# Performance work log

Hardware: AMD Instinct MI355X
Metric: run time of the kernel (lower is better)

Reference implementation:

```python
import jax, jax.numpy as jnp
import numpy as np

SH_DEGREE = 4
SH_DIM = (SH_DEGREE + 1) ** 2  # 25
SCALE_MIN, SCALE_MAX = 0.01, 100.0
SCALE_PCT = 0.1
SRF, GPP = 1, 1


def sh_basis(d):
    # Real spherical harmonics up to l=4 for unit directions d (..., 3) -> (..., 25)
    x, y, z = d[..., 0], d[..., 1], d[..., 2]
    x2, y2, z2 = x * x, y * y, z * z
    return jnp.stack([
        jnp.full_like(x, 0.2820947918),
        0.4886025119 * y, 0.4886025119 * z, 0.4886025119 * x,
        1.0925484306 * x * y, 1.0925484306 * y * z, 0.3153915653 * (3.0 * z2 - 1.0),
        1.0925484306 * x * z, 0.5462742153 * (x2 - y2),
        0.5900435899 * y * (3.0 * x2 - y2), 2.8906114426 * x * y * z,
        0.4570457995 * y * (5.0 * z2 - 1.0), 0.3731763326 * z * (5.0 * z2 - 3.0),
        0.4570457995 * x * (5.0 * z2 - 1.0), 1.4453057213 * z * (x2 - y2),
        0.5900435899 * x * (x2 - 3.0 * y2),
        2.5033429418 * x * y * (x2 - y2), 1.7701307698 * y * z * (3.0 * x2 - y2),
        0.9461746958 * x * y * (7.0 * z2 - 1.0), 0.6690465436 * y * z * (7.0 * z2 - 3.0),
        0.1057855469 * (35.0 * z2 * z2 - 30.0 * z2 + 3.0),
        0.6690465436 * x * z * (7.0 * z2 - 3.0),
        0.4730873479 * (x2 - y2) * (7.0 * z2 - 1.0),
        1.7701307698 * x * z * (x2 - 3.0 * y2),
        0.6258357354 * (x2 * x2 - 6.0 * x2 * y2 + y2 * y2),
    ], -1)


# Fixed sample directions + inverse basis matrices for per-band SH rotation (Wigner-D via sampling)
_rng = np.random.default_rng(0)
_SAMPLES, _YS_INV = {}, {}
for _l in range(1, SH_DEGREE + 1):
    _v = _rng.normal(size=(2 * _l + 1, 3))
    _v /= np.linalg.norm(_v, axis=-1, keepdims=True)
    _SAMPLES[_l] = _v.astype(np.float32)
    _B = np.asarray(sh_basis(jnp.asarray(_SAMPLES[_l])))[:, _l * _l:(_l + 1) ** 2]  # (n, n) rows=samples
    _YS_INV[_l] = np.linalg.inv(_B.T).astype(np.float32)  # inverse of columns-are-samples matrix


def quat_to_rotmat(q):
    # wxyz convention
    w, x, y, z = q[..., 0], q[..., 1], q[..., 2], q[..., 3]
    r0 = jnp.stack([1 - 2 * (y * y + z * z), 2 * (x * y - w * z), 2 * (x * z + w * y)], -1)
    r1 = jnp.stack([2 * (x * y + w * z), 1 - 2 * (x * x + z * z), 2 * (y * z - w * x)], -1)
    r2 = jnp.stack([2 * (x * z - w * y), 2 * (y * z + w * x), 1 - 2 * (x * x + y * y)], -1)
    return jnp.stack([r0, r1, r2], -2)


def rotate_sh(sh, R_c2w):
    # sh: (B,V,R,srf,gpp,3,25); R_c2w: (B,V,3,3). Block-diagonal per-band rotation.
    outs = [sh[..., :1]]  # l=0 invariant
    for l in range(1, SH_DEGREE + 1):
        lo, hi = l * l, (l + 1) ** 2
        S = jnp.asarray(_SAMPLES[l])  # (n,3)
        drot = jnp.einsum('bvji,nj->bvni', R_c2w, S)  # R^T d_n
        Yrot = jnp.swapaxes(sh_basis(drot)[..., lo:hi], -1, -2)  # (B,V,n,n) columns=samples
        D = jnp.swapaxes(Yrot @ jnp.asarray(_YS_INV[l]), -1, -2)  # coefficient rotation
        outs.append(jnp.einsum('bvmn,bvrsgxn->bvrsgxm', D, sh[..., lo:hi]))
    return jnp.concatenate(outs, -1)


def setup_inputs() -> dict:
    key = jax.random.key(0)
    ks = jax.random.split(key, 8)
    B, V, H, W = 2, 4, 256, 256
    R = H * W
    C = 3 + 4 + 3 * SH_DIM  # 82
    pre_gaussians = jax.random.normal(ks[0], (B, V, R, SRF, C), jnp.float32)
    pixel_centers = jax.random.uniform(ks[1], (B, V, R, SRF, 2), jnp.float32)
    q = jax.random.normal(ks[2], (B, V, 4), jnp.float32)
    q = q / jnp.linalg.norm(q, axis=-1, keepdims=True)
    Rm = quat_to_rotmat(q)
    t = 0.5 * jax.random.normal(ks[3], (B, V, 3), jnp.float32)
    E = jnp.zeros((B, V, 4, 4), jnp.float32)
    E = E.at[..., :3, :3].set(Rm).at[..., :3, 3].set(t).at[..., 3, 3].set(1.0)
    f = 1.0 + 0.2 * jax.random.uniform(ks[4], (B, V, 2), jnp.float32)
    c = 0.5 + 0.02 * jax.random.normal(ks[5], (B, V, 2), jnp.float32)
    K = jnp.zeros((B, V, 3, 3), jnp.float32)
    K = K.at[..., 0, 0].set(f[..., 0]).at[..., 1, 1].set(f[..., 1])
    K = K.at[..., 0, 2].set(c[..., 0]).at[..., 1, 2].set(c[..., 1]).at[..., 2, 2].set(1.0)
    opacities = jax.random.uniform(ks[6], (B, V, R), jnp.float32)
    depths = 0.5 + 9.5 * jax.random.uniform(ks[7], (B, V, R), jnp.float32)
    return {"pre_gaussians": pre_gaussians, "pixel_centers": pixel_centers,
            "extrinsics": E, "intrinsics": K, "opacities": opacities,
            "depths": depths, "img_h": H, "img_w": W}


def reference(pre_gaussians, pixel_centers, extrinsics, intrinsics, opacities, depths, img_h, img_w):
    H, W = img_h, img_w
    B, V, R = pre_gaussians.shape[:3]
    C = pre_gaussians.shape[-1]
    pg = jnp.broadcast_to(pre_gaussians[..., None, :], (B, V, R, SRF, GPP, C))
    pc = jnp.broadcast_to(pixel_centers[..., None, :], (B, V, R, SRF, GPP, 2))
    op = jnp.broadcast_to(opacities[..., None, None], (B, V, R, SRF, GPP))
    dep = jnp.broadcast_to(depths[..., None, None], (B, V, R, SRF, GPP))
    scales_raw, quats, sh = pg[..., :3], pg[..., 3:7], pg[..., 7:]
    scales = (SCALE_MIN + (SCALE_MAX - SCALE_MIN) * jax.nn.sigmoid(scales_raw)) * dep[..., None]
    pixel_size = jnp.array([1.0 / W, 1.0 / H], jnp.float32)
    K2inv = jnp.linalg.inv(intrinsics[..., :2, :2])
    scale_adj = SCALE_PCT * jnp.einsum('bvij,j->bv', K2inv, pixel_size)
    scales = scales * scale_adj[:, :, None, None, None, None]
    quats = quats / jnp.linalg.norm(quats, axis=-1, keepdims=True)
    R_w2c = extrinsics[..., :3, :3]
    R_c2w = jnp.swapaxes(R_w2c, -1, -2)
    Rq = quat_to_rotmat(quats)
    cov = jnp.einsum('...ik,...k,...jk->...ij', Rq, scales * scales, Rq)  # Rq S S^T Rq^T
    cov = jnp.einsum('bvai,bvrsgij,bvcj->bvrsgac', R_c2w, cov, R_c2w)
    Kinv = jnp.linalg.inv(intrinsics)
    xy1 = jnp.concatenate([pc, jnp.ones_like(pc[..., :1])], -1)
    dir_cam = jnp.einsum('bvij,bvrsgj->bvrsgi', Kinv, xy1)
    dir_cam = dir_cam / jnp.linalg.norm(dir_cam, axis=-1, keepdims=True)
    ray_d = jnp.einsum('bvij,bvrsgj->bvrsgi', R_c2w, dir_cam)
    t = extrinsics[..., :3, 3]
    cam_o = -jnp.einsum('bvij,bvj->bvi', R_c2w, t)  # camera center in world
    ray_o = jnp.broadcast_to(cam_o[:, :, None, None, None, :], ray_d.shape)
    means = ray_o + ray_d * dep[..., None]
    sh = sh.reshape(B, V, R, SRF, GPP, 3, SH_DIM)
    sh = rotate_sh(sh, R_c2w)
    return (means, scales, cov, quats, op, sh)
```

## Files before the change

kernel.cpp:

```cpp
#include <hip/hip_runtime.h>

#define VSZ  192
#define TILE 64
#define ROWW 95
#define NTHR 256

__device__ __forceinline__ void sh_basis25(float x, float y, float z, float* Y) {
    float x2 = x * x, y2 = y * y, z2 = z * z;
    Y[0]  = 0.2820947918f;
    Y[1]  = 0.4886025119f * y;
    Y[2]  = 0.4886025119f * z;
    Y[3]  = 0.4886025119f * x;
    Y[4]  = 1.0925484306f * x * y;
    Y[5]  = 1.0925484306f * y * z;
    Y[6]  = 0.3153915653f * (3.0f * z2 - 1.0f);
    Y[7]  = 1.0925484306f * x * z;
    Y[8]  = 0.5462742153f * (x2 - y2);
    Y[9]  = 0.5900435899f * y * (3.0f * x2 - y2);
    Y[10] = 2.8906114426f * x * y * z;
    Y[11] = 0.4570457995f * y * (5.0f * z2 - 1.0f);
    Y[12] = 0.3731763326f * z * (5.0f * z2 - 3.0f);
    Y[13] = 0.4570457995f * x * (5.0f * z2 - 1.0f);
    Y[14] = 1.4453057213f * z * (x2 - y2);
    Y[15] = 0.5900435899f * x * (x2 - 3.0f * y2);
    Y[16] = 2.5033429418f * x * y * (x2 - y2);
    Y[17] = 1.7701307698f * y * z * (3.0f * x2 - y2);
    Y[18] = 0.9461746958f * x * y * (7.0f * z2 - 1.0f);
    Y[19] = 0.6690465436f * y * z * (7.0f * z2 - 3.0f);
    Y[20] = 0.1057855469f * (35.0f * z2 * z2 - 30.0f * z2 + 3.0f);
    Y[21] = 0.6690465436f * x * z * (7.0f * z2 - 3.0f);
    Y[22] = 0.4730873479f * (x2 - y2) * (7.0f * z2 - 1.0f);
    Y[23] = 1.7701307698f * x * z * (x2 - 3.0f * y2);
    Y[24] = 0.6258357354f * (x2 * x2 - 6.0f * x2 * y2 + y2 * y2);
}

__global__ __launch_bounds__(64) void setup_kernel(
        const float* __restrict__ ext,
        const float* __restrict__ intr,
        const int* __restrict__ ph,
        const int* __restrict__ pw,
        float* __restrict__ vdg) {
    __shared__ float Bs[24][9];
    __shared__ float Yrs[24][9];
    __shared__ float normInv[24];

    int bv = blockIdx.x;
    int tid = threadIdx.x;
    const float* E = ext + bv * 16;
    const float* K = intr + bv * 9;
    float* o = vdg + bv * VSZ;

    const float z0 = 0.5f, r0 = 0.8660254037844386f;
    const float TWO_PI = 6.283185307179586f;

    if (tid < 24) {
        int l, base;
        if      (tid < 3)  { l = 1; base = 0;  }
        else if (tid < 8)  { l = 2; base = 3;  }
        else if (tid < 15) { l = 3; base = 8;  }
        else               { l = 4; base = 15; }
        int n  = 2 * l + 1;
        int si = tid - base;
        int lo = l * l;
        float phs = 0.4f + TWO_PI * (float)si / (float)n;
        float sx = r0 * cosf(phs), sy = r0 * sinf(phs), sz = z0;
        float Y[25];
        sh_basis25(sx, sy, sz, Y);
        for (int k = 0; k < n; k++) Bs[tid][k] = Y[lo + k];
        float dx = E[0] * sx + E[1] * sy + E[2]  * sz;
        float dy = E[4] * sx + E[5] * sy + E[6]  * sz;
        float dz = E[8] * sx + E[9] * sy + E[10] * sz;
        sh_basis25(dx, dy, dz, Y);
        for (int k = 0; k < n; k++) Yrs[tid][k] = Y[lo + k];
    }
    __syncthreads();

    if (tid < 24) {
        int l, base;
        if      (tid < 3)  { l = 1; base = 0;  }
        else if (tid < 8)  { l = 2; base = 3;  }
        else if (tid < 15) { l = 3; base = 8;  }
        else               { l = 4; base = 15; }
        int n = 2 * l + 1;
        int m = tid - base;
        float acc = 0.f;
        for (int s = 0; s < n; s++) { float v = Bs[base + s][m]; acc += v * v; }
        normInv[tid] = 1.0f / acc;
    }
    __syncthreads();

    const int dofs[5] = {0, 22, 31, 56, 105};
    for (int e = tid; e < 164; e += 64) {
        int l, ebase, sbase;
        if      (e < 9)  { l = 1; ebase = 0;  sbase = 0;  }
        else if (e < 34) { l = 2; ebase = 9;  sbase = 3;  }
        else if (e < 83) { l = 3; ebase = 34; sbase = 8;  }
        else             { l = 4; ebase = 83; sbase = 15; }
        int n = 2 * l + 1;
        int el = e - ebase;
        int m = el / n, k = el % n;
        float acc = 0.f;
        for (int s = 0; s < n; s++) acc += Yrs[sbase + s][k] * Bs[sbase + s][m];
        o[dofs[l] + m * n + k] = acc * normInv[sbase + m];
    }

    if (tid == 0) {
        float Rw2c[3][3], Rc2w[3][3], t[3];
        for (int i = 0; i < 3; i++) {
            for (int j = 0; j < 3; j++) Rw2c[i][j] = E[i * 4 + j];
            t[i] = E[i * 4 + 3];
        }
        for (int i = 0; i < 3; i++)
            for (int j = 0; j < 3; j++) Rc2w[i][j] = Rw2c[j][i];
        for (int i = 0; i < 3; i++)
            for (int j = 0; j < 3; j++) o[i * 3 + j] = Rc2w[i][j];
        for (int i = 0; i < 3; i++) {
            float s = 0.f;
            for (int j = 0; j < 3; j++) s += Rc2w[i][j] * t[j];
            o[9 + i] = -s;
        }
        float a = K[0], b = K[1], c = K[2], d = K[3], e = K[4], f = K[5],
              g = K[6], h = K[7], ii = K[8];
        float det = a * (e * ii - f * h) - b * (d * ii - f * g) + c * (d * h - e * g);
        float id = 1.0f / det;
        o[12 + 0] = (e * ii - f * h) * id; o[12 + 1] = (c * h - b * ii) * id; o[12 + 2] = (b * f - c * e) * id;
        o[12 + 3] = (f * g - d * ii) * id; o[12 + 4] = (a * ii - c * g) * id; o[12 + 5] = (c * d - a * f) * id;
        o[12 + 6] = (d * h - e * g) * id; o[12 + 7] = (b * g - a * h) * id; o[12 + 8] = (a * e - b * d) * id;
        float det2 = a * e - b * d;
        float i00 = e / det2, i01 = -b / det2, i10 = -d / det2, i11 = a / det2;
        float ps0 = 1.0f / (float)(*pw), ps1 = 1.0f / (float)(*ph);
        o[21] = 0.1f * ((i00 + i10) * ps0 + (i01 + i11) * ps1);
    }
}

template <int NB>
__device__ __forceinline__ void apply_D(const float* __restrict__ D,
                                        const float* __restrict__ si,
                                        float* __restrict__ so) {
#pragma unroll
    for (int m = 0; m < NB; m++) {
        float acc = 0.f;
#pragma unroll
        for (int k = 0; k < NB; k++) acc += D[m * NB + k] * si[k];
        so[m] = acc;
    }
}

template <int W>
__device__ __forceinline__ void copy_sec(const float* __restrict__ lds,
                                         float* __restrict__ dst,
                                         int cb, int cnt) {
    for (int e = threadIdx.x; e < cnt * W; e += NTHR) {
        int r = e / W, c = e - r * W;
        dst[e] = lds[r * ROWW + cb + c];
    }
}

__global__ __launch_bounds__(NTHR, 6) void adapter_kernel(
    const float* __restrict__ pg, const float* __restrict__ pc,
    const float* __restrict__ ops, const float* __restrict__ deps,
    const float* __restrict__ vdg, float* __restrict__ out,
    int R, long long N)
{
    __shared__ float tile[TILE * ROWW];
    __shared__ float vd[VSZ];

    int bv = blockIdx.y;
    long long tilebase = (long long)bv * R + (long long)blockIdx.x * TILE;
    int cnt = R - blockIdx.x * TILE;
    if (cnt > TILE) cnt = TILE;

    for (int i = threadIdx.x; i < 186; i += NTHR) vd[i] = vdg[bv * VSZ + i];

    const float* src = pg + tilebase * 82;
    for (int ff = threadIdx.x; ff < cnt * 82; ff += NTHR) {
        int rr = ff / 82, cc = ff - rr * 82;
        tile[rr * ROWW + cc] = src[ff];
    }
    __syncthreads();

    int rec = threadIdx.x & 63;
    int sub = threadIdx.x >> 6;
    bool active = rec < cnt;
    long long g = tilebase + rec;
    float* row = tile + rec * ROWW;

    float gin[7];
    float depth = 0.f, opac = 0.f, px = 0.f, py = 0.f;
    float si[25];

    if (sub == 0) {
        if (active) {
#pragma unroll
            for (int i = 0; i < 7; i++) gin[i] = row[i];
            depth = deps[g];
            opac  = ops[g];
            float2 pxy = ((const float2*)pc)[g];
            px = pxy.x; py = pxy.y;
        }
    } else {
        if (active) {
            int cb = 7 + 25 * (sub - 1);
#pragma unroll
            for (int m = 0; m < 25; m++) si[m] = row[cb + m];
        }
    }
    __syncthreads();

    if (sub == 0) {
        if (active) {
            float sadj = vd[21];
            float sc[3];
#pragma unroll
            for (int i = 0; i < 3; i++) {
                float sg = 1.0f / (1.0f + expf(-gin[i]));
                sc[i] = (0.01f + 99.99f * sg) * depth * sadj;
            }
            float qw = gin[3], qx = gin[4], qy = gin[5], qz = gin[6];
            float qn = rsqrtf(qw * qw + qx * qx + qy * qy + qz * qz);
            qw *= qn; qx *= qn; qy *= qn; qz *= qn;
            float Rq[3][3];
            Rq[0][0] = 1.f - 2.f * (qy * qy + qz * qz);
            Rq[0][1] = 2.f * (qx * qy - qw * qz);
            Rq[0][2] = 2.f * (qx * qz + qw * qy);
            Rq[1][0] = 2.f * (qx * qy + qw * qz);
            Rq[1][1] = 1.f - 2.f * (qx * qx + qz * qz);
            Rq[1][2] = 2.f * (qy * qz - qw * qx);
            Rq[2][0] = 2.f * (qx * qz - qw * qy);
            Rq[2][1] = 2.f * (qy * qz + qw * qx);
            Rq[2][2] = 1.f - 2.f * (qx * qx + qy * qy);

            float Rc[3][3];
#pragma unroll
            for (int i = 0; i < 3; i++)
#pragma unroll
                for (int j = 0; j < 3; j++) Rc[i][j] = vd[i * 3 + j];

            float A[3][3];
#pragma unroll
            for (int i = 0; i < 3; i++)
#pragma unroll
                for (int k = 0; k < 3; k++)
                    A[i][k] = Rc[i][0] * Rq[0][k] + Rc[i][1] * Rq[1][k] + Rc[i][2] * Rq[2][k];
            float s2[3] = {sc[0] * sc[0], sc[1] * sc[1], sc[2] * sc[2]};

            float dx = vd[12] * px + vd[13] * py + vd[14];
            float dy = vd[15] * px + vd[16] * py + vd[17];
            float dz = vd[18] * px + vd[19] * py + vd[20];
            float dn = rsqrtf(dx * dx + dy * dy + dz * dz);
            dx *= dn; dy *= dn; dz *= dn;
            float rdx = Rc[0][0] * dx + Rc[0][1] * dy + Rc[0][2] * dz;
            float rdy = Rc[1][0] * dx + Rc[1][1] * dy + Rc[1][2] * dz;
            float rdz = Rc[2][0] * dx + Rc[2][1] * dy + Rc[2][2] * dz;

            row[0] = vd[9]  + rdx * depth;
            row[1] = vd[10] + rdy * depth;
            row[2] = vd[11] + rdz * depth;
            row[3] = sc[0]; row[4] = sc[1]; row[5] = sc[2];
#pragma unroll
            for (int i = 0; i < 3; i++)
#pragma unroll
                for (int j = 0; j < 3; j++)
                    row[6 + i * 3 + j] = A[i][0] * s2[0] * A[j][0] + A[i][1] * s2[1] * A[j][1] + A[i][2] * s2[2] * A[j][2];
            row[15] = qw; row[16] = qx; row[17] = qy; row[18] = qz;
            row[19] = opac;
        }
    } else {
        if (active) {
            float so[25];
            so[0] = si[0];
            apply_D<3>(vd + 22,  si + 1,  so + 1);
            apply_D<5>(vd + 31,  si + 4,  so + 4);
            apply_D<7>(vd + 56,  si + 9,  so + 9);
            apply_D<9>(vd + 105, si + 16, so + 16);
            int ob = 20 + 25 * (sub - 1);
#pragma unroll
            for (int m = 0; m < 25; m++) row[ob + m] = so[m];
        }
    }
    __syncthreads();

    copy_sec<3>(tile,  out +           3 * tilebase, 0,  cnt);
    copy_sec<3>(tile,  out +  3 * N +  3 * tilebase, 3,  cnt);
    copy_sec<9>(tile,  out +  6 * N +  9 * tilebase, 6,  cnt);
    copy_sec<4>(tile,  out + 15 * N +  4 * tilebase, 15, cnt);
    copy_sec<1>(tile,  out + 19 * N +      tilebase, 19, cnt);
    copy_sec<75>(tile, out + 20 * N + 75 * tilebase, 20, cnt);
}

extern "C" void kernel_launch(void* const* d_in, const int* in_sizes, int n_in,
                              void* d_out, int out_size, void* d_ws, size_t ws_size,
                              hipStream_t stream) {
    const float* pg   = (const float*)d_in[0];
    const float* pc   = (const float*)d_in[1];
    const float* ext  = (const float*)d_in[2];
    const float* intr = (const float*)d_in[3];
    const float* ops  = (const float*)d_in[4];
    const float* dep  = (const float*)d_in[5];
    const int*   ph   = (const int*)d_in[6];
    const int*   pw   = (const int*)d_in[7];

    int BV = in_sizes[2] / 16;
    long long N = (long long)in_sizes[4];
    int R = (int)(N / BV);

    float* vd = (float*)d_ws;
    setup_kernel<<<BV, 64, 0, stream>>>(ext, intr, ph, pw, vd);

    dim3 grid((R + TILE - 1) / TILE, BV);
    adapter_kernel<<<grid, NTHR, 0, stream>>>(pg, pc, ops, dep, vd, (float*)d_out, R, N);
}
```

Before: 93.99 us.

## Vectorize global tile loads and stores via section-packed LDS output layout

Replaces the padded per-record LDS row layout with a packed input copy followed by separate contiguous output sections (means, scales, cov, quats, opacity, SH) laid out exactly like the global output. Full tiles then use float4 global loads and float4 global stores with no per-element division/modulo indexing. Partial tiles keep a scalar path. The float4 path assumes 16-byte alignment of each section's tile base, which only holds for suitable R and N. Output sections also overwrite LDS space that held other records' inputs, so correctness depends on all inputs being in registers before the writes begin.

```diff
diff --git a/kernel.cpp b/kernel.cpp
--- a/kernel.cpp
+++ b/kernel.cpp
@@ -2,8 +2,15 @@
 
 #define VSZ  192
 #define TILE 64
-#define ROWW 95
 #define NTHR 256
+#define IN_F  (TILE * 82)
+#define SEC_M  0
+#define SEC_S  192
+#define SEC_C  384
+#define SEC_Q  960
+#define SEC_O  1216
+#define SEC_SH 1280
+#define OUT_F  6080
 
 __device__ __forceinline__ void sh_basis25(float x, float y, float z, float* Y) {
     float x2 = x * x, y2 = y * y, z2 = z * z;
@@ -146,36 +153,30 @@
     }
 }
 
-template <int W>
-__device__ __forceinline__ void copy_sec(const float* __restrict__ lds,
-                                         float* __restrict__ dst,
-                                         int cb, int cnt) {
-    for (int e = threadIdx.x; e < cnt * W; e += NTHR) {
-        int r = e / W, c = e - r * W;
-        dst[e] = lds[r * ROWW + cb + c];
-    }
-}
-
 __global__ __launch_bounds__(NTHR, 6) void adapter_kernel(
     const float* __restrict__ pg, const float* __restrict__ pc,
     const float* __restrict__ ops, const float* __restrict__ deps,
     const float* __restrict__ vdg, float* __restrict__ out,
     int R, long long N)
 {
-    __shared__ float tile[TILE * ROWW];
+    __shared__ __align__(16) float tile[OUT_F];
     __shared__ float vd[VSZ];
 
     int bv = blockIdx.y;
     long long tilebase = (long long)bv * R + (long long)blockIdx.x * TILE;
     int cnt = R - blockIdx.x * TILE;
     if (cnt > TILE) cnt = TILE;
+    bool full = (cnt == TILE);
 
     for (int i = threadIdx.x; i < 186; i += NTHR) vd[i] = vdg[bv * VSZ + i];
 
     const float* src = pg + tilebase * 82;
-    for (int ff = threadIdx.x; ff < cnt * 82; ff += NTHR) {
-        int rr = ff / 82, cc = ff - rr * 82;
-        tile[rr * ROWW + cc] = src[ff];
+    if (full) {
+        const float4* s4 = (const float4*)src;
+        float4* t4 = (float4*)tile;
+        for (int e = threadIdx.x; e < IN_F / 4; e += NTHR) t4[e] = s4[e];
+    } else {
+        for (int ff = threadIdx.x; ff < cnt * 82; ff += NTHR) tile[ff] = src[ff];
     }
     __syncthreads();
 
@@ -183,7 +184,7 @@
     int sub = threadIdx.x >> 6;
     bool active = rec < cnt;
     long long g = tilebase + rec;
-    float* row = tile + rec * ROWW;
+    const float* row = tile + rec * 82;
 
     float gin[7];
     float depth = 0.f, opac = 0.f, px = 0.f, py = 0.f;
@@ -253,17 +254,20 @@
             float rdy = Rc[1][0] * dx + Rc[1][1] * dy + Rc[1][2] * dz;
             float rdz = Rc[2][0] * dx + Rc[2][1] * dy + Rc[2][2] * dz;
 
-            row[0] = vd[9]  + rdx * depth;
-            row[1] = vd[10] + rdy * depth;
-            row[2] = vd[11] + rdz * depth;
-            row[3] = sc[0]; row[4] = sc[1]; row[5] = sc[2];
+            tile[SEC_M + 3 * rec + 0] = vd[9]  + rdx * depth;
+            tile[SEC_M + 3 * rec + 1] = vd[10] + rdy * depth;
+            tile[SEC_M + 3 * rec + 2] = vd[11] + rdz * depth;
+            tile[SEC_S + 3 * rec + 0] = sc[0];
+            tile[SEC_S + 3 * rec + 1] = sc[1];
+            tile[SEC_S + 3 * rec + 2] = sc[2];
 #pragma unroll
             for (int i = 0; i < 3; i++)
 #pragma unroll
                 for (int j = 0; j < 3; j++)
-                    row[6 + i * 3 + j] = A[i][0] * s2[0] * A[j][0] + A[i][1] * s2[1] * A[j][1] + A[i][2] * s2[2] * A[j][2];
-            row[15] = qw; row[16] = qx; row[17] = qy; row[18] = qz;
-            row[19] = opac;
+                    tile[SEC_C + 9 * rec + i * 3 + j] =
+                        A[i][0] * s2[0] * A[j][0] + A[i][1] * s2[1] * A[j][1] + A[i][2] * s2[2] * A[j][2];
+            ((float4*)(tile + SEC_Q))[rec] = make_float4(qw, qx, qy, qz);
+            tile[SEC_O + rec] = opac;
         }
     } else {
         if (active) {
@@ -273,19 +277,43 @@
             apply_D<5>(vd + 31,  si + 4,  so + 4);
             apply_D<7>(vd + 56,  si + 9,  so + 9);
             apply_D<9>(vd + 105, si + 16, so + 16);
-            int ob = 20 + 25 * (sub - 1);
-#pragma unroll
-            for (int m = 0; m < 25; m++) row[ob + m] = so[m];
-        }
-    }
-    __syncthreads();
-
-    copy_sec<3>(tile,  out +           3 * tilebase, 0,  cnt);
-    copy_sec<3>(tile,  out +  3 * N +  3 * tilebase, 3,  cnt);
-    copy_sec<9>(tile,  out +  6 * N +  9 * tilebase, 6,  cnt);
-    copy_sec<4>(tile,  out + 15 * N +  4 * tilebase, 15, cnt);
-    copy_sec<1>(tile,  out + 19 * N +      tilebase, 19, cnt);
-    copy_sec<75>(tile, out + 20 * N + 75 * tilebase, 20, cnt);
+            float* dstsh = tile + SEC_SH + 75 * rec + 25 * (sub - 1);
+#pragma unroll
+            for (int m = 0; m < 25; m++) dstsh[m] = so[m];
+        }
+    }
+    __syncthreads();
+
+    if (full) {
+        const float4* t4 = (const float4*)tile;
+        float4* dm  = (float4*)(out +           3 * tilebase);
+        float4* ds  = (float4*)(out +  3 * N +  3 * tilebase);
+        float4* dc  = (float4*)(out +  6 * N +  9 * tilebase);
+        float4* dq  = (float4*)(out + 15 * N +  4 * tilebase);
+        float4* dop = (float4*)(out + 19 * N +      tilebase);
+        float4* dsh = (float4*)(out + 20 * N + 75 * tilebase);
+        int tid = threadIdx.x;
+        if (tid < 48)  dm[tid]  = t4[SEC_M / 4 + tid];
+        if (tid < 48)  ds[tid]  = t4[SEC_S / 4 + tid];
+        for (int e = tid; e < 144; e += NTHR) dc[e] = t4[SEC_C / 4 + e];
+        if (tid < 64)  dq[tid]  = t4[SEC_Q / 4 + tid];
+        if (tid < 16)  dop[tid] = t4[SEC_O / 4 + tid];
+        for (int e = tid; e < 1200; e += NTHR) dsh[e] = t4[SEC_SH / 4 + e];
+    } else {
+        int tid = threadIdx.x;
+        float* dm  = out +           3 * tilebase;
+        float* ds  = out +  3 * N +  3 * tilebase;
+        float* dc  = out +  6 * N +  9 * tilebase;
+        float* dq  = out + 15 * N +  4 * tilebase;
+        float* dop = out + 19 * N +      tilebase;
+        float* dsh = out + 20 * N + 75 * tilebase;
+        for (int e = tid; e < cnt * 3;  e += NTHR) dm[e]  = tile[SEC_M + e];
+        for (int e = tid; e < cnt * 3;  e += NTHR) ds[e]  = tile[SEC_S + e];
+        for (int e = tid; e < cnt * 9;  e += NTHR) dc[e]  = tile[SEC_C + e];
+        for (int e = tid; e < cnt * 4;  e += NTHR) dq[e]  = tile[SEC_Q + e];
+        for (int e = tid; e < cnt;      e += NTHR) dop[e] = tile[SEC_O + e];
+        for (int e = tid; e < cnt * 75; e += NTHR) dsh[e] = tile[SEC_SH + e];
+    }
 }
 
 extern "C" void kernel_launch(void* const* d_in, const int* in_sizes, int n_in,
```

Result: no change. 93.84 us (-0.2%).

## Make each wavefront process its own 16-record tile without block barriers

Applied to the files above, without the earlier changes.

Splits the 64-record block tile into four independent per-wavefront windows of 16 records, so every __syncthreads can be removed. Full windows are loaded with 16-byte global_load_lds direct-to-LDS transfers. Outputs are staged per section in LDS and written back as vectorized non-temporal float4 stores, with a scalar fallback for partial tiles. Each wave loads its own copy of the per-view constants, which adds redundant work. The direct-to-LDS path relies on 16-byte alignment of the record base, which holds only when the per-view record count is a multiple of 16.

```diff
diff --git a/kernel.cpp b/kernel.cpp
--- a/kernel.cpp
+++ b/kernel.cpp
@@ -1,9 +1,24 @@
 #include <hip/hip_runtime.h>
-
-#define VSZ  192
-#define TILE 64
-#define ROWW 95
-#define NTHR 256
+#include <stdint.h>
+
+#define VSZ   192
+#define NTHR  256
+#define WRECS 16
+#define WIN_F (WRECS * 82)
+#define WV_F  1520
+#define WM  0
+#define WS  48
+#define WC  96
+#define WQ  240
+#define WO  304
+#define WSH 320
+
+typedef float vf4 __attribute__((ext_vector_type(4)));
+typedef const __attribute__((address_space(1))) uint32_t* gas_ptr;
+typedef __attribute__((address_space(3))) uint32_t* las_ptr;
+__device__ __forceinline__ void g2lds16(const float4* g, float4* l) {
+    __builtin_amdgcn_global_load_lds((gas_ptr)(const void*)g, (las_ptr)(void*)l, 16, 0, 0);
+}
 
 __device__ __forceinline__ void sh_basis25(float x, float y, float z, float* Y) {
     float x2 = x * x, y2 = y * y, z2 = z * z;
@@ -146,77 +161,73 @@
     }
 }
 
-template <int W>
-__device__ __forceinline__ void copy_sec(const float* __restrict__ lds,
-                                         float* __restrict__ dst,
-                                         int cb, int cnt) {
-    for (int e = threadIdx.x; e < cnt * W; e += NTHR) {
-        int r = e / W, c = e - r * W;
-        dst[e] = lds[r * ROWW + cb + c];
-    }
-}
-
 __global__ __launch_bounds__(NTHR, 6) void adapter_kernel(
     const float* __restrict__ pg, const float* __restrict__ pc,
     const float* __restrict__ ops, const float* __restrict__ deps,
     const float* __restrict__ vdg, float* __restrict__ out,
     int R, long long N)
 {
-    __shared__ float tile[TILE * ROWW];
+    __shared__ __align__(16) float lds[4 * WV_F];
     __shared__ float vd[VSZ];
 
-    int bv = blockIdx.y;
-    long long tilebase = (long long)bv * R + (long long)blockIdx.x * TILE;
-    int cnt = R - blockIdx.x * TILE;
-    if (cnt > TILE) cnt = TILE;
-
-    for (int i = threadIdx.x; i < 186; i += NTHR) vd[i] = vdg[bv * VSZ + i];
-
-    const float* src = pg + tilebase * 82;
-    for (int ff = threadIdx.x; ff < cnt * 82; ff += NTHR) {
-        int rr = ff / 82, cc = ff - rr * 82;
-        tile[rr * ROWW + cc] = src[ff];
-    }
-    __syncthreads();
-
-    int rec = threadIdx.x & 63;
-    int sub = threadIdx.x >> 6;
+    int lane = threadIdx.x & 63;
+    int wid  = threadIdx.x >> 6;
+    int bv   = blockIdx.y;
+
+    for (int i = lane; i < 186; i += 64) vd[i] = vdg[bv * VSZ + i];
+
+    int r0 = blockIdx.x * (4 * WRECS) + wid * WRECS;
+    int cnt = R - r0; if (cnt > WRECS) cnt = WRECS;
+    if (cnt <= 0) return;
+    float* W = lds + wid * WV_F;
+    long long gb = (long long)bv * R + r0;
+
+    const float* src = pg + gb * 82;
+    if (cnt == WRECS) {
+        const float4* s4 = (const float4*)src;
+        float4* d4 = (float4*)W;
+#pragma unroll
+        for (int k = 0; k < 5; k++) g2lds16(s4 + k * 64 + lane, d4 + k * 64 + lane);
+        if (lane < 8) g2lds16(s4 + 320 + lane, d4 + 320 + lane);
+    } else {
+        for (int f = lane; f < cnt * 82; f += 64) W[f] = src[f];
+    }
+    asm volatile("s_waitcnt vmcnt(0)" ::: "memory");
+    __builtin_amdgcn_sched_barrier(0);
+
+    int rec  = lane & 15;
+    int role = lane >> 4;
     bool active = rec < cnt;
-    long long g = tilebase + rec;
-    float* row = tile + rec * ROWW;
-
-    float gin[7];
+    long long g = gb + rec;
+    const float* row = W + rec * 82;
+
+    float rin[25];
     float depth = 0.f, opac = 0.f, px = 0.f, py = 0.f;
-    float si[25];
-
-    if (sub == 0) {
-        if (active) {
-#pragma unroll
-            for (int i = 0; i < 7; i++) gin[i] = row[i];
+    if (active) {
+        if (role == 0) {
+#pragma unroll
+            for (int i = 0; i < 7; i++) rin[i] = row[i];
             depth = deps[g];
             opac  = ops[g];
             float2 pxy = ((const float2*)pc)[g];
             px = pxy.x; py = pxy.y;
+        } else {
+            int cb = 7 + 25 * (role - 1);
+#pragma unroll
+            for (int m = 0; m < 25; m++) rin[m] = row[cb + m];
         }
-    } else {
-        if (active) {
-            int cb = 7 + 25 * (sub - 1);
-#pragma unroll
-            for (int m = 0; m < 25; m++) si[m] = row[cb + m];
-        }
-    }
-    __syncthreads();
-
-    if (sub == 0) {
-        if (active) {
+    }
+
+    if (active) {
+        if (role == 0) {
             float sadj = vd[21];
             float sc[3];
 #pragma unroll
             for (int i = 0; i < 3; i++) {
-                float sg = 1.0f / (1.0f + expf(-gin[i]));
+                float sg = 1.0f / (1.0f + expf(-rin[i]));
                 sc[i] = (0.01f + 99.99f * sg) * depth * sadj;
             }
-            float qw = gin[3], qx = gin[4], qy = gin[5], qz = gin[6];
+            float qw = rin[3], qx = rin[4], qy = rin[5], qz = rin[6];
             float qn = rsqrtf(qw * qw + qx * qx + qy * qy + qz * qz);
             qw *= qn; qx *= qn; qy *= qn; qz *= qn;
             float Rq[3][3];
@@ -253,39 +264,64 @@
             float rdy = Rc[1][0] * dx + Rc[1][1] * dy + Rc[1][2] * dz;
             float rdz = Rc[2][0] * dx + Rc[2][1] * dy + Rc[2][2] * dz;
 
-            row[0] = vd[9]  + rdx * depth;
-            row[1] = vd[10] + rdy * depth;
-            row[2] = vd[11] + rdz * depth;
-            row[3] = sc[0]; row[4] = sc[1]; row[5] = sc[2];
+            W[WM + 3 * rec + 0] = vd[9]  + rdx * depth;
+            W[WM + 3 * rec + 1] = vd[10] + rdy * depth;
+            W[WM + 3 * rec + 2] = vd[11] + rdz * depth;
+            W[WS + 3 * rec + 0] = sc[0];
+            W[WS + 3 * rec + 1] = sc[1];
+            W[WS + 3 * rec + 2] = sc[2];
 #pragma unroll
             for (int i = 0; i < 3; i++)
 #pragma unroll
                 for (int j = 0; j < 3; j++)
-                    row[6 + i * 3 + j] = A[i][0] * s2[0] * A[j][0] + A[i][1] * s2[1] * A[j][1] + A[i][2] * s2[2] * A[j][2];
-            row[15] = qw; row[16] = qx; row[17] = qy; row[18] = qz;
-            row[19] = opac;
+                    W[WC + 9 * rec + i * 3 + j] =
+                        A[i][0] * s2[0] * A[j][0] + A[i][1] * s2[1] * A[j][1] + A[i][2] * s2[2] * A[j][2];
+            ((float4*)(W + WQ))[rec] = make_float4(qw, qx, qy, qz);
+            W[WO + rec] = opac;
+        } else {
+            float so[25];
+            so[0] = rin[0];
+            apply_D<3>(vd + 22,  rin + 1,  so + 1);
+            apply_D<5>(vd + 31,  rin + 4,  so + 4);
+            apply_D<7>(vd + 56,  rin + 9,  so + 9);
+            apply_D<9>(vd + 105, rin + 16, so + 16);
+            float* dstsh = W + WSH + 75 * rec + 25 * (role - 1);
+#pragma unroll
+            for (int m = 0; m < 25; m++) dstsh[m] = so[m];
         }
+    }
+
+    if (cnt == WRECS) {
+        const vf4* w4 = (const vf4*)W;
+        vf4* dm  = (vf4*)(out +           3 * gb);
+        vf4* dsc = (vf4*)(out +  3 * N +  3 * gb);
+        vf4* dc  = (vf4*)(out +  6 * N +  9 * gb);
+        vf4* dq  = (vf4*)(out + 15 * N +  4 * gb);
+        vf4* dop = (vf4*)(out + 19 * N +      gb);
+        vf4* dsh = (vf4*)(out + 20 * N + 75 * gb);
+        if (lane < 12) __builtin_nontemporal_store(w4[WM / 4 + lane], dm + lane);
+        if (lane < 12) __builtin_nontemporal_store(w4[WS / 4 + lane], dsc + lane);
+        if (lane < 36) __builtin_nontemporal_store(w4[WC / 4 + lane], dc + lane);
+        if (lane < 16) __builtin_nontemporal_store(w4[WQ / 4 + lane], dq + lane);
+        if (lane < 4)  __builtin_nontemporal_store(w4[WO / 4 + lane], dop + lane);
+#pragma unroll
+        for (int k = 0; k < 4; k++)
+            __builtin_nontemporal_store(w4[WSH / 4 + k * 64 + lane], dsh + k * 64 + lane);
+        if (lane < 44) __builtin_nontemporal_store(w4[WSH / 4 + 256 + lane], dsh + 256 + lane);
     } else {
-        if (active) {
-            float so[25];
-            so[0] = si[0];
-            apply_D<3>(vd + 22,  si + 1,  so + 1);
-            apply_D<5>(vd + 31,  si + 4,  so + 4);
-            apply_D<7>(vd + 56,  si + 9,  so + 9);
-            apply_D<9>(vd + 105, si + 16, so + 16);
-            int ob = 20 + 25 * (sub - 1);
-#pragma unroll
-            for (int m = 0; m < 25; m++) row[ob + m] = so[m];
-        }
-    }
-    __syncthreads();
-
-    copy_sec<3>(tile,  out +           3 * tilebase, 0,  cnt);
-    copy_sec<3>(tile,  out +  3 * N +  3 * tilebase, 3,  cnt);
-    copy_sec<9>(tile,  out +  6 * N +  9 * tilebase, 6,  cnt);
-    copy_sec<4>(tile,  out + 15 * N +  4 * tilebase, 15, cnt);
-    copy_sec<1>(tile,  out + 19 * N +      tilebase, 19, cnt);
-    copy_sec<75>(tile, out + 20 * N + 75 * tilebase, 20, cnt);
+        float* dm  = out +           3 * gb;
+        float* dsc = out +  3 * N +  3 * gb;
+        float* dc  = out +  6 * N +  9 * gb;
+        float* dq  = out + 15 * N +  4 * gb;
+        float* dop = out + 19 * N +      gb;
+        float* dsh = out + 20 * N + 75 * gb;
+        for (int e = lane; e < cnt * 3;  e += 64) __builtin_nontemporal_store(W[WM + e], dm + e);
+        for (int e = lane; e < cnt * 3;  e += 64) __builtin_nontemporal_store(W[WS + e], dsc + e);
+        for (int e = lane; e < cnt * 9;  e += 64) __builtin_nontemporal_store(W[WC + e], dc + e);
+        for (int e = lane; e < cnt * 4;  e += 64) __builtin_nontemporal_store(W[WQ + e], dq + e);
+        for (int e = lane; e < cnt;      e += 64) __builtin_nontemporal_store(W[WO + e], dop + e);
+        for (int e = lane; e < cnt * 75; e += 64) __builtin_nontemporal_store(W[WSH + e], dsh + e);
+    }
 }
 
 extern "C" void kernel_launch(void* const* d_in, const int* in_sizes, int n_in,
@@ -307,6 +343,6 @@
     float* vd = (float*)d_ws;
     setup_kernel<<<BV, 64, 0, stream>>>(ext, intr, ph, pw, vd);
 
-    dim3 grid((R + TILE - 1) / TILE, BV);
+    dim3 grid((R + 63) / 64, BV);
     adapter_kernel<<<grid, NTHR, 0, stream>>>(pg, pc, ops, dep, vd, (float*)d_out, R, N);
 }
```

Measured after the change: 79.53 us. 15.4% less time.
